# Kernel tuning notes

Measured on AMD Instinct MI355X. Metric: run time of the kernel, lower is better.

Reference implementation:

```python
import jax, jax.numpy as jnp
import numpy as np

B, T, D, H = 4, 2048, 2048, 16
HD = D // H  # 128
EPS = 1e-5


def setup_inputs() -> dict:
    key = jax.random.key(0)
    ks = jax.random.split(key, 16)
    s_in = 1.0 / np.sqrt(D)
    s_ff = 1.0 / np.sqrt(4 * D)
    return {
        "x": jax.random.normal(ks[0], (B, T, D), jnp.float32),
        # per-head q/k/v projections stacked over heads: [H, D, HD]
        "Wq": jax.random.normal(ks[1], (H, D, HD), jnp.float32) * s_in,
        "bq": jnp.zeros((H, HD), jnp.float32),
        "Wk": jax.random.normal(ks[2], (H, D, HD), jnp.float32) * s_in,
        "bk": jnp.zeros((H, HD), jnp.float32),
        "Wv": jax.random.normal(ks[3], (H, D, HD), jnp.float32) * s_in,
        "bv": jnp.zeros((H, HD), jnp.float32),
        # feed-forward
        "W1": jax.random.normal(ks[4], (D, 4 * D), jnp.float32) * s_in,
        "b1": jnp.zeros((4 * D,), jnp.float32),
        "W2": jax.random.normal(ks[5], (4 * D, D), jnp.float32) * s_ff,
        "b2": jnp.zeros((D,), jnp.float32),
        # layer norms
        "g1": jnp.ones((D,), jnp.float32),
        "be1": jnp.zeros((D,), jnp.float32),
        "g2": jnp.ones((D,), jnp.float32),
        "be2": jnp.zeros((D,), jnp.float32),
    }


def _layernorm(x, g, b):
    mu = jnp.mean(x, axis=-1, keepdims=True)
    var = jnp.mean(jnp.square(x - mu), axis=-1, keepdims=True)
    return (x - mu) * jax.lax.rsqrt(var + EPS) * g + b


def reference(x, Wq, bq, Wk, bk, Wv, bv, W1, b1, W2, b2, g1, be1, g2, be2):
    h = _layernorm(x, g1, be1)
    # per-head projections: [B, H, T, HD]
    q = jnp.einsum("btd,hde->bhte", h, Wq) + bq[None, :, None, :]
    k = jnp.einsum("btd,hde->bhte", h, Wk) + bk[None, :, None, :]
    v = jnp.einsum("btd,hde->bhte", h, Wv) + bv[None, :, None, :]
    scale = 1.0 / jnp.sqrt(jnp.asarray(HD, q.dtype))
    logits = jnp.einsum("bhte,bhse->bhts", q, k) * scale  # [B,H,T,T]
    causal = jnp.tril(jnp.ones((T, T), bool))
    logits = jnp.where(causal[None, None], logits, -jnp.inf)
    attn = jax.nn.softmax(logits, axis=-1)
    out = jnp.einsum("bhts,bhse->bhte", attn, v)  # [B,H,T,HD]
    # concat heads in head order -> [B,T,D]
    out = out.transpose(0, 2, 1, 3).reshape(B, T, D)
    x = x + out
    h2 = _layernorm(x, g2, be2)
    ff = jax.nn.relu(h2 @ W1 + b1) @ W2 + b2
    return x + ff
```

## Files before the change

kernel.cpp:

```cpp
#include <hip/hip_runtime.h>
#include <stdint.h>

#define TLEN 2048
#define DDIM 2048
#define NHEAD 16
#define HDIM 128
#define BSZ 4

typedef short bf16x8 __attribute__((ext_vector_type(8)));
typedef float f32x4 __attribute__((ext_vector_type(4)));

__device__ __forceinline__ unsigned short f32_bf16(float f) {
  union { float f; unsigned int u; } v; v.f = f;
  unsigned int u = v.u;
  unsigned int r = (u + 0x7fffu + ((u >> 16) & 1u)) >> 16;
  return (unsigned short)r;
}

__device__ __forceinline__ void async_cp16(const void* g, void* l) {
  __builtin_amdgcn_global_load_lds(
      (const __attribute__((address_space(1))) unsigned int*)g,
      (__attribute__((address_space(3))) unsigned int*)l, 16, 0, 0);
}

__global__ __launch_bounds__(256) void transpose_bf16_kernel(
    const float* __restrict__ in, unsigned short* __restrict__ out,
    int R, int C, long in_z, long out_z) {
  __shared__ float tile[32][33];
  in += (long)blockIdx.z * in_z;
  out += (long)blockIdx.z * out_z;
  int c0 = blockIdx.x * 32, r0 = blockIdx.y * 32;
  int cr = threadIdx.x & 31, rr = threadIdx.x >> 5;
#pragma unroll
  for (int i = 0; i < 4; ++i)
    tile[rr + i * 8][cr] = in[(long)(r0 + rr + i * 8) * C + c0 + cr];
  __syncthreads();
#pragma unroll
  for (int i = 0; i < 4; ++i)
    out[(long)(c0 + rr + i * 8) * R + r0 + cr] = f32_bf16(tile[cr][rr + i * 8]);
}

__device__ __forceinline__ void block_reduce2(float& s, float& q) {
#pragma unroll
  for (int off = 32; off >= 1; off >>= 1) {
    s += __shfl_xor(s, off);
    q += __shfl_xor(q, off);
  }
  __shared__ float rs[4], rq[4];
  int lane = threadIdx.x & 63, wid = threadIdx.x >> 6;
  if (lane == 0) { rs[wid] = s; rq[wid] = q; }
  __syncthreads();
  s = rs[0] + rs[1] + rs[2] + rs[3];
  q = rq[0] + rq[1] + rq[2] + rq[3];
}

__global__ __launch_bounds__(256) void ln_kernel(
    const float* __restrict__ x, const float* __restrict__ g,
    const float* __restrict__ be, unsigned short* __restrict__ hb) {
  int row = blockIdx.x, tid = threadIdx.x;
  const float* xr = x + (long)row * DDIM;
  float4 v0 = *(const float4*)(xr + tid * 4);
  float4 v1 = *(const float4*)(xr + 1024 + tid * 4);
  float s = v0.x + v0.y + v0.z + v0.w + v1.x + v1.y + v1.z + v1.w;
  float q = v0.x * v0.x + v0.y * v0.y + v0.z * v0.z + v0.w * v0.w +
            v1.x * v1.x + v1.y * v1.y + v1.z * v1.z + v1.w * v1.w;
  block_reduce2(s, q);
  float mu = s * (1.0f / DDIM);
  float var = q * (1.0f / DDIM) - mu * mu;
  float rstd = rsqrtf(var + 1e-5f);
  float4 g0 = *(const float4*)(g + tid * 4);
  float4 g1v = *(const float4*)(g + 1024 + tid * 4);
  float4 b0 = *(const float4*)(be + tid * 4);
  float4 b1v = *(const float4*)(be + 1024 + tid * 4);
  ushort4 o0, o1;
  o0.x = f32_bf16((v0.x - mu) * rstd * g0.x + b0.x);
  o0.y = f32_bf16((v0.y - mu) * rstd * g0.y + b0.y);
  o0.z = f32_bf16((v0.z - mu) * rstd * g0.z + b0.z);
  o0.w = f32_bf16((v0.w - mu) * rstd * g0.w + b0.w);
  o1.x = f32_bf16((v1.x - mu) * rstd * g1v.x + b1v.x);
  o1.y = f32_bf16((v1.y - mu) * rstd * g1v.y + b1v.y);
  o1.z = f32_bf16((v1.z - mu) * rstd * g1v.z + b1v.z);
  o1.w = f32_bf16((v1.w - mu) * rstd * g1v.w + b1v.w);
  *(ushort4*)(hb + (long)row * DDIM + tid * 4) = o0;
  *(ushort4*)(hb + (long)row * DDIM + 1024 + tid * 4) = o1;
}

__global__ __launch_bounds__(256) void resid_ln_kernel(
    const float* __restrict__ x, float* xa,
    const float* __restrict__ g, const float* __restrict__ be,
    unsigned short* __restrict__ hb) {
  int row = blockIdx.x, tid = threadIdx.x;
  const float* xr = x + (long)row * DDIM;
  float* ar = xa + (long)row * DDIM;
  float4 v0 = *(const float4*)(xr + tid * 4);
  float4 a0 = *(const float4*)(ar + tid * 4);
  float4 v1 = *(const float4*)(xr + 1024 + tid * 4);
  float4 a1 = *(const float4*)(ar + 1024 + tid * 4);
  v0.x += a0.x; v0.y += a0.y; v0.z += a0.z; v0.w += a0.w;
  v1.x += a1.x; v1.y += a1.y; v1.z += a1.z; v1.w += a1.w;
  *(float4*)(ar + tid * 4) = v0;
  *(float4*)(ar + 1024 + tid * 4) = v1;
  float s = v0.x + v0.y + v0.z + v0.w + v1.x + v1.y + v1.z + v1.w;
  float q = v0.x * v0.x + v0.y * v0.y + v0.z * v0.z + v0.w * v0.w +
            v1.x * v1.x + v1.y * v1.y + v1.z * v1.z + v1.w * v1.w;
  block_reduce2(s, q);
  float mu = s * (1.0f / DDIM);
  float var = q * (1.0f / DDIM) - mu * mu;
  float rstd = rsqrtf(var + 1e-5f);
  float4 g0 = *(const float4*)(g + tid * 4);
  float4 g1v = *(const float4*)(g + 1024 + tid * 4);
  float4 b0 = *(const float4*)(be + tid * 4);
  float4 b1v = *(const float4*)(be + 1024 + tid * 4);
  ushort4 o0, o1;
  o0.x = f32_bf16((v0.x - mu) * rstd * g0.x + b0.x);
  o0.y = f32_bf16((v0.y - mu) * rstd * g0.y + b0.y);
  o0.z = f32_bf16((v0.z - mu) * rstd * g0.z + b0.z);
  o0.w = f32_bf16((v0.w - mu) * rstd * g0.w + b0.w);
  o1.x = f32_bf16((v1.x - mu) * rstd * g1v.x + b1v.x);
  o1.y = f32_bf16((v1.y - mu) * rstd * g1v.y + b1v.y);
  o1.z = f32_bf16((v1.z - mu) * rstd * g1v.z + b1v.z);
  o1.w = f32_bf16((v1.w - mu) * rstd * g1v.w + b1v.w);
  *(ushort4*)(hb + (long)row * DDIM + tid * 4) = o0;
  *(ushort4*)(hb + (long)row * DDIM + 1024 + tid * 4) = o1;
}

__device__ __forceinline__ void gemm_core(const unsigned short* __restrict__ A,
                                          const unsigned short* __restrict__ Bt,
                                          int K, int m0, int n0,
                                          f32x4 acc[4][4]) {
  __shared__ unsigned short sA[128 * 64];
  __shared__ unsigned short sB[128 * 64];
  const int tid = threadIdx.x;
  const int lane = tid & 63, wid = tid >> 6;
  const int wm = (wid & 1) * 64, wn = (wid >> 1) * 64;
  const int lm = lane & 15, lq = lane >> 4;
#pragma unroll
  for (int mi = 0; mi < 4; ++mi)
#pragma unroll
    for (int ni = 0; ni < 4; ++ni)
      acc[mi][ni] = (f32x4){0.f, 0.f, 0.f, 0.f};
  const int rbase = wid * 32;
  const int ri = lane >> 3;
  const int kgl = lane & 7;
  const int nk = K >> 6;
  for (int kt = 0; kt < nk; ++kt) {
    const unsigned short* Ak = A + (long)m0 * K + (long)kt * 64;
    const unsigned short* Bk = Bt + (long)n0 * K + (long)kt * 64;
#pragma unroll
    for (int ins = 0; ins < 4; ++ins) {
      int row = rbase + ins * 8 + ri;
      int kg = kgl ^ (row & 7);
      async_cp16(Ak + (long)row * K + kg * 8, &sA[(rbase + ins * 8) * 64]);
      async_cp16(Bk + (long)row * K + kg * 8, &sB[(rbase + ins * 8) * 64]);
    }
    __syncthreads();
#pragma unroll
    for (int kc = 0; kc < 2; ++kc) {
      bf16x8 af[4], bfr[4];
#pragma unroll
      for (int mi = 0; mi < 4; ++mi) {
        int row = wm + mi * 16 + lm;
        int kg = (kc * 4 + lq) ^ (row & 7);
        af[mi] = *(const bf16x8*)(&sA[row * 64 + kg * 8]);
      }
#pragma unroll
      for (int ni = 0; ni < 4; ++ni) {
        int row = wn + ni * 16 + lm;
        int kg = (kc * 4 + lq) ^ (row & 7);
        bfr[ni] = *(const bf16x8*)(&sB[row * 64 + kg * 8]);
      }
#pragma unroll
      for (int mi = 0; mi < 4; ++mi)
#pragma unroll
        for (int ni = 0; ni < 4; ++ni)
          acc[mi][ni] = __builtin_amdgcn_mfma_f32_16x16x32_bf16(af[mi], bfr[ni], acc[mi][ni], 0, 0, 0);
    }
    __syncthreads();
  }
}

__global__ __launch_bounds__(256) void gemm_qkv_kernel(
    const unsigned short* __restrict__ A, const unsigned short* __restrict__ WT,
    unsigned short* __restrict__ Qb, unsigned short* __restrict__ Kb,
    unsigned short* __restrict__ VTb,
    const float* __restrict__ bq, const float* __restrict__ bk,
    const float* __restrict__ bv) {
  int m0 = blockIdx.x * 128, n0 = blockIdx.y * 128;
  int z = blockIdx.z;
  const unsigned short* Bt = WT + (long)z * DDIM * DDIM;
  f32x4 acc[4][4];
  gemm_core(A, Bt, DDIM, m0, n0, acc);
  const float* bias = (z == 0) ? bq : (z == 1) ? bk : bv;
  int lane = threadIdx.x & 63, wid = threadIdx.x >> 6;
  int wm = (wid & 1) * 64, wn = (wid >> 1) * 64, lm = lane & 15, lq = lane >> 4;
  int h = n0 >> 7;
#pragma unroll
  for (int mi = 0; mi < 4; ++mi) {
    int rowb = m0 + wm + mi * 16 + lq * 4;
    int b = rowb >> 11, t0 = rowb & (TLEN - 1);
#pragma unroll
    for (int ni = 0; ni < 4; ++ni) {
      int col = n0 + wn + ni * 16 + lm;
      int e = col & (HDIM - 1);
      float bsv = bias[col];
      if (z < 2) {
        unsigned short* o = (z == 0) ? Qb : Kb;
        long base = ((long)(b * NHEAD + h) * TLEN + t0) * HDIM + e;
#pragma unroll
        for (int r = 0; r < 4; ++r)
          o[base + (long)r * HDIM] = f32_bf16(acc[mi][ni][r] + bsv);
      } else {
        long base = ((long)(b * NHEAD + h) * HDIM + e) * TLEN + t0;
        ushort4 pk;
        pk.x = f32_bf16(acc[mi][ni][0] + bsv);
        pk.y = f32_bf16(acc[mi][ni][1] + bsv);
        pk.z = f32_bf16(acc[mi][ni][2] + bsv);
        pk.w = f32_bf16(acc[mi][ni][3] + bsv);
        *(ushort4*)(VTb + base) = pk;
      }
    }
  }
}

template <int MODE>
__global__ __launch_bounds__(256) void gemm_ffn_kernel(
    const unsigned short* __restrict__ A, const unsigned short* __restrict__ Bt,
    void* __restrict__ outv, const float* __restrict__ bias, int K, int N) {
  int m0 = blockIdx.x * 128, n0 = blockIdx.y * 128;
  f32x4 acc[4][4];
  gemm_core(A, Bt, K, m0, n0, acc);
  int lane = threadIdx.x & 63, wid = threadIdx.x >> 6;
  int wm = (wid & 1) * 64, wn = (wid >> 1) * 64, lm = lane & 15, lq = lane >> 4;
#pragma unroll
  for (int mi = 0; mi < 4; ++mi) {
    int rowb = m0 + wm + mi * 16 + lq * 4;
#pragma unroll
    for (int ni = 0; ni < 4; ++ni) {
      int col = n0 + wn + ni * 16 + lm;
      float bsv = bias[col];
#pragma unroll
      for (int r = 0; r < 4; ++r) {
        long idx = (long)(rowb + r) * N + col;
        float v = acc[mi][ni][r] + bsv;
        if (MODE == 0) {
          ((unsigned short*)outv)[idx] = f32_bf16(v > 0.f ? v : 0.f);
        } else {
          float* o = (float*)outv;
          o[idx] = o[idx] + v;
        }
      }
    }
  }
}

__global__ __launch_bounds__(256, 3) void attn_kernel(
    const unsigned short* __restrict__ Qb, const unsigned short* __restrict__ Kb,
    const unsigned short* __restrict__ VTb, float* __restrict__ Ob) {
  __shared__ __align__(16) char smem[49152];
  unsigned short* kbuf0 = (unsigned short*)smem;
  unsigned short* kbuf1 = (unsigned short*)(smem + 16384);
  unsigned short* sV = (unsigned short*)(smem + 32768);
  const int tid = threadIdx.x, lane = tid & 63, wid = tid >> 6;
  const int lm = lane & 15, lq = lane >> 4;
  int flat = blockIdx.x;
  int swz = (flat & 7) * 256 + (flat >> 3);
  int m5 = swz & 31;
  int bxx = (m5 & 1) ? (m5 >> 1) : (31 - (m5 >> 1));
  int h = (swz >> 5) & 15;
  int b = swz >> 9;
  const int q0 = bxx * 64;
  const long bh = (long)(b * NHEAD + h);
  const unsigned short* qp = Qb + (bh * TLEN + q0 + wid * 16) * HDIM;
  const unsigned short* kp = Kb + bh * TLEN * HDIM;
  const unsigned short* vp = VTb + bh * HDIM * TLEN;
  bf16x8 qf[4];
#pragma unroll
  for (int c = 0; c < 4; ++c)
    qf[c] = *(const bf16x8*)(qp + (long)lm * HDIM + c * 32 + lq * 8);
  f32x4 oacc[8];
#pragma unroll
  for (int c = 0; c < 8; ++c) oacc[c] = (f32x4){0.f, 0.f, 0.f, 0.f};
  float mr[4], lr[4];
#pragma unroll
  for (int r = 0; r < 4; ++r) { mr[r] = -3.0e38f; lr[r] = 0.f; }
  const float sl = 0.08838834764831845f * 1.4426950408889634f;
  const int nk = bxx + 1;
  const int kri = lane >> 4, krg = lane & 15;
  const int vri = lane >> 3, vrg = lane & 7;
#pragma unroll
  for (int i = 0; i < 4; ++i) {
    int row = wid * 16 + i * 4 + kri;
    async_cp16(kp + (long)row * HDIM + (krg ^ (row & 7)) * 8,
               kbuf0 + (wid * 16 + i * 4) * 128);
  }
  for (int it = 0; it < nk; ++it) {
    const int kb = it * 64;
    unsigned short* kc_ = (it & 1) ? kbuf1 : kbuf0;
    unsigned short* kn_ = (it & 1) ? kbuf0 : kbuf1;
    __asm__ volatile("s_waitcnt vmcnt(0)" ::: "memory");
    __asm__ volatile("s_barrier" ::: "memory");
#pragma unroll
    for (int i = 0; i < 4; ++i) {
      int row = wid * 32 + i * 8 + vri;
      async_cp16(vp + (long)row * TLEN + kb + (vrg ^ (row & 7)) * 8,
                 sV + (wid * 32 + i * 8) * 64);
    }
    if (it + 1 < nk) {
      const unsigned short* kp1 = kp + (long)(kb + 64) * HDIM;
#pragma unroll
      for (int i = 0; i < 4; ++i) {
        int row = wid * 16 + i * 4 + kri;
        async_cp16(kp1 + (long)row * HDIM + (krg ^ (row & 7)) * 8,
                   kn_ + (wid * 16 + i * 4) * 128);
      }
    }
    f32x4 s[4];
#pragma unroll
    for (int ni = 0; ni < 4; ++ni) s[ni] = (f32x4){0.f, 0.f, 0.f, 0.f};
    __builtin_amdgcn_s_setprio(1);
#pragma unroll
    for (int c = 0; c < 4; ++c) {
      bf16x8 bk[4];
#pragma unroll
      for (int ni = 0; ni < 4; ++ni) {
        int row = ni * 16 + lm;
        int g = (c * 4 + lq) ^ (row & 7);
        bk[ni] = *(const bf16x8*)(&kc_[row * 128 + g * 8]);
      }
#pragma unroll
      for (int ni = 0; ni < 4; ++ni)
        s[ni] = __builtin_amdgcn_mfma_f32_16x16x32_bf16(qf[c], bk[ni], s[ni], 0, 0, 0);
    }
    __builtin_amdgcn_s_setprio(0);
    const bool diag = (it == nk - 1);
    float v[4][4], mx[4];
#pragma unroll
    for (int r = 0; r < 4; ++r) {
      int qrow = q0 + wid * 16 + lq * 4 + r;
      float m = -3.0e38f;
#pragma unroll
      for (int ni = 0; ni < 4; ++ni) {
        float t = s[ni][r] * sl;
        if (diag && (kb + ni * 16 + lm > qrow)) t = -3.0e38f;
        v[r][ni] = t;
        m = fmaxf(m, t);
      }
#pragma unroll
      for (int off = 8; off >= 1; off >>= 1) m = fmaxf(m, __shfl_xor(m, off));
      mx[r] = m;
    }
    bool grew = (mx[0] > mr[0]) | (mx[1] > mr[1]) | (mx[2] > mr[2]) | (mx[3] > mr[3]);
    if (__any(grew)) {
#pragma unroll
      for (int r = 0; r < 4; ++r) {
        float mn = fmaxf(mr[r], mx[r]);
        float a = exp2f(mr[r] - mn);
        mr[r] = mn;
        lr[r] *= a;
#pragma unroll
        for (int c = 0; c < 8; ++c) oacc[c][r] *= a;
      }
    }
    float p[4][4];
#pragma unroll
    for (int r = 0; r < 4; ++r) {
      float rs = 0.f;
#pragma unroll
      for (int ni = 0; ni < 4; ++ni) {
        p[r][ni] = exp2f(v[r][ni] - mr[r]);
        rs += p[r][ni];
      }
      lr[r] += rs;
    }
    if (it + 1 < nk) {
      __asm__ volatile("s_waitcnt vmcnt(4)" ::: "memory");
    } else {
      __asm__ volatile("s_waitcnt vmcnt(0)" ::: "memory");
    }
    __asm__ volatile("s_barrier" ::: "memory");
    unsigned short* pw = kc_ + wid * 1024;
#pragma unroll
    for (int r = 0; r < 4; ++r) {
      int prow = lq * 4 + r;
#pragma unroll
      for (int ni = 0; ni < 4; ++ni)
        pw[prow * 64 + ((ni * 16 + lm) ^ ((prow & 7) << 3))] = f32_bf16(p[r][ni]);
    }
    __asm__ volatile("s_waitcnt lgkmcnt(0)" ::: "memory");
    __builtin_amdgcn_sched_barrier(0);
    __builtin_amdgcn_s_setprio(1);
#pragma unroll
    for (int kc = 0; kc < 2; ++kc) {
      bf16x8 pf = *(const bf16x8*)(&pw[lm * 64 + ((kc * 32 + lq * 8) ^ ((lm & 7) << 3))]);
#pragma unroll
      for (int c = 0; c < 8; ++c) {
        int row = c * 16 + lm;
        int g = (kc * 4 + lq) ^ (row & 7);
        bf16x8 vf = *(const bf16x8*)(&sV[row * 64 + g * 8]);
        oacc[c] = __builtin_amdgcn_mfma_f32_16x16x32_bf16(pf, vf, oacc[c], 0, 0, 0);
      }
    }
    __builtin_amdgcn_s_setprio(0);
  }
  __syncthreads();
#pragma unroll
  for (int r = 0; r < 4; ++r) {
#pragma unroll
    for (int off = 8; off >= 1; off >>= 1) lr[r] += __shfl_xor(lr[r], off);
  }
  float inv[4];
#pragma unroll
  for (int r = 0; r < 4; ++r) inv[r] = 1.f / lr[r];
  float* sO = (float*)smem;
#pragma unroll
  for (int c = 0; c < 8; ++c)
#pragma unroll
    for (int r = 0; r < 4; ++r)
      sO[(wid * 16 + lq * 4 + r) * 132 + c * 16 + lm] = oacc[c][r] * inv[r];
  __syncthreads();
  float* ob = Ob + ((long)b * TLEN + q0) * DDIM + (long)h * HDIM;
#pragma unroll
  for (int i = 0; i < 8; ++i) {
    int idx = i * 256 + tid;
    int row = idx >> 5, c4 = (idx & 31) * 4;
    *(float4*)(ob + (long)row * DDIM + c4) = *(const float4*)(&sO[row * 132 + c4]);
  }
}

extern "C" void kernel_launch(void* const* d_in, const int* in_sizes, int n_in,
                              void* d_out, int out_size, void* d_ws, size_t ws_size,
                              hipStream_t stream) {
  const float* x   = (const float*)d_in[0];
  const float* Wq  = (const float*)d_in[1];
  const float* bq  = (const float*)d_in[2];
  const float* Wk  = (const float*)d_in[3];
  const float* bk  = (const float*)d_in[4];
  const float* Wv  = (const float*)d_in[5];
  const float* bv  = (const float*)d_in[6];
  const float* W1  = (const float*)d_in[7];
  const float* b1  = (const float*)d_in[8];
  const float* W2  = (const float*)d_in[9];
  const float* b2  = (const float*)d_in[10];
  const float* g1  = (const float*)d_in[11];
  const float* be1 = (const float*)d_in[12];
  const float* g2  = (const float*)d_in[13];
  const float* be2 = (const float*)d_in[14];
  float* out = (float*)d_out;
  char* ws = (char*)d_ws;
  unsigned short* wtqkv  = (unsigned short*)(ws + 0L);
  unsigned short* qb     = (unsigned short*)(ws + 25165824L);
  unsigned short* kbuf   = (unsigned short*)(ws + 58720256L);
  unsigned short* vtb    = (unsigned short*)(ws + 92274688L);
  unsigned short* hbf    = (unsigned short*)(ws + 125829120L);
  unsigned short* ff1buf = qb;
  unsigned short* wt1    = kbuf;
  unsigned short* wt2    = vtb;

  dim3 blk(256);
  transpose_bf16_kernel<<<dim3(4, 64, 16), blk, 0, stream>>>(Wq, wtqkv, 2048, 128, 2048L * 128, 2048L * 128);
  transpose_bf16_kernel<<<dim3(4, 64, 16), blk, 0, stream>>>(Wk, wtqkv + 2048L * 2048, 2048, 128, 2048L * 128, 2048L * 128);
  transpose_bf16_kernel<<<dim3(4, 64, 16), blk, 0, stream>>>(Wv, wtqkv + 2L * 2048 * 2048, 2048, 128, 2048L * 128, 2048L * 128);

  ln_kernel<<<dim3(8192), blk, 0, stream>>>(x, g1, be1, hbf);
  gemm_qkv_kernel<<<dim3(64, 16, 3), blk, 0, stream>>>(hbf, wtqkv, qb, kbuf, vtb, bq, bk, bv);
  attn_kernel<<<dim3(2048), blk, 0, stream>>>(qb, kbuf, vtb, out);

  transpose_bf16_kernel<<<dim3(256, 64, 1), blk, 0, stream>>>(W1, wt1, 2048, 8192, 0, 0);
  transpose_bf16_kernel<<<dim3(64, 256, 1), blk, 0, stream>>>(W2, wt2, 8192, 2048, 0, 0);

  resid_ln_kernel<<<dim3(8192), blk, 0, stream>>>(x, out, g2, be2, hbf);

  for (int c = 0; c < 4; ++c) {
    gemm_ffn_kernel<0><<<dim3(16, 64), blk, 0, stream>>>(
        hbf + (long)c * 2048 * DDIM, wt1, ff1buf, b1, DDIM, 4 * DDIM);
    gemm_ffn_kernel<1><<<dim3(16, 16), blk, 0, stream>>>(
        ff1buf, wt2, out + (long)c * 2048 * DDIM, b2, 4 * DDIM, DDIM);
  }
}
```

Measured before the change: 1.717 ms.

## Split FFN over hidden dimension and lazily rescale attention softmax

```diff
diff --git a/kernel.cpp b/kernel.cpp
--- a/kernel.cpp
+++ b/kernel.cpp
@@ -126,7 +126,7 @@
 
 __device__ __forceinline__ void gemm_core(const unsigned short* __restrict__ A,
                                           const unsigned short* __restrict__ Bt,
-                                          int K, int m0, int n0,
+                                          int K, int lda, int ldb, int m0, int n0,
                                           f32x4 acc[4][4]) {
   __shared__ unsigned short sA[128 * 64];
   __shared__ unsigned short sB[128 * 64];
@@ -144,14 +144,14 @@
   const int kgl = lane & 7;
   const int nk = K >> 6;
   for (int kt = 0; kt < nk; ++kt) {
-    const unsigned short* Ak = A + (long)m0 * K + (long)kt * 64;
-    const unsigned short* Bk = Bt + (long)n0 * K + (long)kt * 64;
+    const unsigned short* Ak = A + (long)m0 * lda + (long)kt * 64;
+    const unsigned short* Bk = Bt + (long)n0 * ldb + (long)kt * 64;
 #pragma unroll
     for (int ins = 0; ins < 4; ++ins) {
       int row = rbase + ins * 8 + ri;
       int kg = kgl ^ (row & 7);
-      async_cp16(Ak + (long)row * K + kg * 8, &sA[(rbase + ins * 8) * 64]);
-      async_cp16(Bk + (long)row * K + kg * 8, &sB[(rbase + ins * 8) * 64]);
+      async_cp16(Ak + (long)row * lda + kg * 8, &sA[(rbase + ins * 8) * 64]);
+      async_cp16(Bk + (long)row * ldb + kg * 8, &sB[(rbase + ins * 8) * 64]);
     }
     __syncthreads();
 #pragma unroll
@@ -189,7 +189,7 @@
   int z = blockIdx.z;
   const unsigned short* Bt = WT + (long)z * DDIM * DDIM;
   f32x4 acc[4][4];
-  gemm_core(A, Bt, DDIM, m0, n0, acc);
+  gemm_core(A, Bt, DDIM, DDIM, DDIM, m0, n0, acc);
   const float* bias = (z == 0) ? bq : (z == 1) ? bk : bv;
   int lane = threadIdx.x & 63, wid = threadIdx.x >> 6;
   int wm = (wid & 1) * 64, wn = (wid >> 1) * 64, lm = lane & 15, lq = lane >> 4;
@@ -225,10 +225,11 @@
 template <int MODE>
 __global__ __launch_bounds__(256) void gemm_ffn_kernel(
     const unsigned short* __restrict__ A, const unsigned short* __restrict__ Bt,
-    void* __restrict__ outv, const float* __restrict__ bias, int K, int N) {
+    void* __restrict__ outv, const float* __restrict__ bias,
+    int K, int lda, int ldb, int N) {
   int m0 = blockIdx.x * 128, n0 = blockIdx.y * 128;
   f32x4 acc[4][4];
-  gemm_core(A, Bt, K, m0, n0, acc);
+  gemm_core(A, Bt, K, lda, ldb, m0, n0, acc);
   int lane = threadIdx.x & 63, wid = threadIdx.x >> 6;
   int wm = (wid & 1) * 64, wn = (wid >> 1) * 64, lm = lane & 15, lq = lane >> 4;
 #pragma unroll
@@ -237,7 +238,7 @@
 #pragma unroll
     for (int ni = 0; ni < 4; ++ni) {
       int col = n0 + wn + ni * 16 + lm;
-      float bsv = bias[col];
+      float bsv = (MODE == 2) ? 0.f : bias[col];
 #pragma unroll
       for (int r = 0; r < 4; ++r) {
         long idx = (long)(rowb + r) * N + col;
@@ -333,7 +334,7 @@
     }
     __builtin_amdgcn_s_setprio(0);
     const bool diag = (it == nk - 1);
-    float v[4][4], mx[4];
+    float v[4][4], pmax[4];
 #pragma unroll
     for (int r = 0; r < 4; ++r) {
       int qrow = q0 + wid * 16 + lq * 4 + r;
@@ -345,15 +346,17 @@
         v[r][ni] = t;
         m = fmaxf(m, t);
       }
-#pragma unroll
-      for (int off = 8; off >= 1; off >>= 1) m = fmaxf(m, __shfl_xor(m, off));
-      mx[r] = m;
-    }
-    bool grew = (mx[0] > mr[0]) | (mx[1] > mr[1]) | (mx[2] > mr[2]) | (mx[3] > mr[3]);
-    if (__any(grew)) {
+      pmax[r] = m;
+    }
+    bool need = (pmax[0] > mr[0] + 8.f) | (pmax[1] > mr[1] + 8.f) |
+                (pmax[2] > mr[2] + 8.f) | (pmax[3] > mr[3] + 8.f);
+    if (__any(need)) {
 #pragma unroll
       for (int r = 0; r < 4; ++r) {
-        float mn = fmaxf(mr[r], mx[r]);
+        float m = pmax[r];
+#pragma unroll
+        for (int off = 8; off >= 1; off >>= 1) m = fmaxf(m, __shfl_xor(m, off));
+        float mn = fmaxf(mr[r], m);
         float a = exp2f(mr[r] - mn);
         mr[r] = mn;
         lr[r] *= a;
@@ -470,10 +473,16 @@
 
   resid_ln_kernel<<<dim3(8192), blk, 0, stream>>>(x, out, g2, be2, hbf);
 
-  for (int c = 0; c < 4; ++c) {
-    gemm_ffn_kernel<0><<<dim3(16, 64), blk, 0, stream>>>(
-        hbf + (long)c * 2048 * DDIM, wt1, ff1buf, b1, DDIM, 4 * DDIM);
-    gemm_ffn_kernel<1><<<dim3(16, 16), blk, 0, stream>>>(
-        ff1buf, wt2, out + (long)c * 2048 * DDIM, b2, 4 * DDIM, DDIM);
-  }
-}
+  for (int s = 0; s < 4; ++s) {
+    gemm_ffn_kernel<0><<<dim3(64, 16), blk, 0, stream>>>(
+        hbf, wt1 + (long)s * 2048 * 2048, ff1buf, b1 + s * 2048,
+        2048, 2048, 2048, 2048);
+    if (s == 0) {
+      gemm_ffn_kernel<1><<<dim3(64, 16), blk, 0, stream>>>(
+          ff1buf, wt2 + (long)s * 2048, out, b2, 2048, 2048, 8192, 2048);
+    } else {
+      gemm_ffn_kernel<2><<<dim3(64, 16), blk, 0, stream>>>(
+          ff1buf, wt2 + (long)s * 2048, out, b2, 2048, 2048, 8192, 2048);
+    }
+  }
+}
```

Result: faster. 1.527 ms (-11.1%).
